# Optimization experiments

Hardware: AMD Instinct MI355X
Metric: run time of the kernel (lower is better)

Reference implementation:

```python
import jax, jax.numpy as jnp
import numpy as np

TAU = 2.0       # init_tau
VTH = 1.0       # v_threshold
VRESET = 0.0    # v_reset (hard reset)
ALPHA = 2.0     # ATan surrogate width
H = 8           # num_heads
W = 20          # attention_window
TIME_STEP = 2   # config.time_step -> global_scale uses 1000 // time_step


@jax.custom_vjp
def spike(x):
    return (x >= 0.0).astype(x.dtype)

def _spike_fwd(x):
    return (x >= 0.0).astype(x.dtype), x

def _spike_bwd(x, g):
    # ATan surrogate gradient (spikingjelly default)
    sg = (ALPHA / 2.0) / (1.0 + (jnp.pi / 2.0 * ALPHA * x) ** 2)
    return (g * sg,)

spike.defvjp(_spike_fwd, _spike_bwd)


def lif(x_seq):
    """Multi-step LIF, decay_input=False, hard reset. x_seq: [T, ...] -> spikes [T, ...]."""
    def step(v, x):
        h = v - (v - VRESET) / TAU + x          # neuronal charge (decay_input=False)
        s = spike(h - VTH)
        v_new = s * VRESET + (1.0 - s) * h      # hard reset
        return v_new, s
    _, s_seq = jax.lax.scan(step, jnp.zeros_like(x_seq[0]), x_seq)
    return s_seq


def bn(x, gamma, beta, eps=1e-5):
    # BatchNorm1d step_mode='m': stats over (T, B) per channel (training-mode stats)
    mean = x.mean(axis=(0, 1))
    var = x.var(axis=(0, 1))
    return (x - mean) * jax.lax.rsqrt(var + eps) * gamma + beta


def _shift(a, o):
    # a: [B, H, T, D]; out[..., t, :] = a[..., t + o, :], zero outside -> local band
    if o == 0:
        return a
    B_, H_, T_, D_ = a.shape
    z = jnp.zeros((B_, H_, abs(o), D_), a.dtype)
    if o > 0:
        return jnp.concatenate([a[:, :, o:, :], z], axis=2)
    return jnp.concatenate([z, a[:, :, :o, :]], axis=2)


def _forward(x, wq, wk, wv, w_mattn, w_proj, w_dw, w_pw, bn_gamma, bn_beta):
    T, B, C = x.shape
    D = C // H
    local_scale = 1.0 / np.sqrt(D * (2 * W + 1)).astype(np.float32)
    global_scale = 1.0 / np.sqrt(D * (1000 // TIME_STEP)).astype(np.float32)

    # spiking QKV: pointwise conv (kernel 1) + BN + LIF
    q = lif(bn(jnp.einsum('tbc,dc->tbd', x, wq), bn_gamma[0], bn_beta[0]))
    k = lif(bn(jnp.einsum('tbc,dc->tbd', x, wk), bn_gamma[1], bn_beta[1]))
    v = lif(bn(jnp.einsum('tbc,dc->tbd', x, wv), bn_gamma[2], bn_beta[2]))

    heads = lambda a: a.reshape(T, B, H, D).transpose(1, 2, 0, 3)   # [B,H,T,D]
    unheads = lambda a: a.transpose(2, 0, 1, 3).reshape(T, B, C)    # [T,B,C]
    qh, kh, vh = heads(q), heads(k), heads(v)

    # global spiking self-attention (no softmax): (Q K^T) V * global_scale
    attn = jnp.einsum('bhtd,bhsd->bhts', qh, kh)
    g_spk = lif(unheads(jnp.einsum('bhts,bhsd->bhtd', attn, vh) * global_scale))

    # local sliding-window attention over offsets [-W, W] (banded, no [T,T] matrix)
    out_l = jnp.zeros_like(vh)
    for o in range(-W, W + 1):
        s = jnp.einsum('bhtd,bhtd->bht', qh, _shift(kh, o))
        out_l = out_l + s[..., None] * _shift(vh, o)
    l_spk = lif(unheads(out_l * local_scale))

    # depthwise temporal conv branch on V: v_dw -> LIF -> v_pw (1x1 over heads)
    dw = jax.lax.conv_general_dilated(
        vh, w_dw, window_strides=(1, 1), padding=((4, 4), (0, 0)),
        dimension_numbers=('NCHW', 'OIHW', 'NCHW'), feature_group_count=H)
    dw_spk_h = heads(lif(unheads(dw)))
    dw_out = unheads(jnp.einsum('bhtd,gh->bgtd', dw_spk_h, w_pw))

    # merge branches, then mattn conv+BN+LIF and proj conv+BN+LIF
    y0 = lif(g_spk + l_spk + dw_out)
    y1 = lif(bn(jnp.einsum('tbc,dc->tbd', y0, w_mattn), bn_gamma[3], bn_beta[3]))
    out = lif(bn(jnp.einsum('tbc,dc->tbd', y1, w_proj), bn_gamma[4], bn_beta[4]))
    return out


def setup_inputs() -> dict:
    key = jax.random.key(0)
    ks = jax.random.split(key, 10)
    T, B, C = 500, 8, 512
    sc = 0.03
    x = jax.random.normal(ks[0], (T, B, C), jnp.float32)
    wq = jax.random.normal(ks[1], (C, C), jnp.float32) * sc
    wk = jax.random.normal(ks[2], (C, C), jnp.float32) * sc
    wv = jax.random.normal(ks[3], (C, C), jnp.float32) * sc
    w_mattn = jax.random.normal(ks[4], (C, C), jnp.float32) * sc
    w_proj = jax.random.normal(ks[5], (C, C), jnp.float32) * sc
    w_dw = jax.random.normal(ks[6], (H, 1, 9, 1), jnp.float32) * 0.3   # depthwise (9,1)
    w_pw = jax.random.normal(ks[7], (H, H), jnp.float32) * 0.3         # 1x1 over heads
    bn_gamma = jax.random.uniform(ks[8], (5, C), jnp.float32) + 0.5
    bn_beta = jax.random.normal(ks[9], (5, C), jnp.float32) * 0.1
    return {'x': x, 'wq': wq, 'wk': wk, 'wv': wv, 'w_mattn': w_mattn,
            'w_proj': w_proj, 'w_dw': w_dw, 'w_pw': w_pw,
            'bn_gamma': bn_gamma, 'bn_beta': bn_beta}


def reference(x, wq, wk, wv, w_mattn, w_proj, w_dw, w_pw, bn_gamma, bn_beta):
    return _forward(x, wq, wk, wv, w_mattn, w_proj, w_dw, w_pw, bn_gamma, bn_beta)
```

## Files before the change

### kernel.cpp

```cpp
#include <hip/hip_runtime.h>
#include <cmath>

#define TT 500
#define NTOT 2048000
#define WW 20

typedef _Float16 f16x8 __attribute__((ext_vector_type(8)));
typedef _Float16 f16x4 __attribute__((ext_vector_type(4)));
typedef float f32x4 __attribute__((ext_vector_type(4)));

#define C1SC 4.8828125e-4f
#define C2SC 2.384185791015625e-7f

__device__ __forceinline__ void gload16(const _Float16* g, _Float16* l) {
    __builtin_amdgcn_global_load_lds(
        (const __attribute__((address_space(1))) unsigned int*)g,
        (__attribute__((address_space(3))) unsigned int*)l, 16, 0, 0);
}
__device__ __forceinline__ void gload16f(const float* g, float* l) {
    __builtin_amdgcn_global_load_lds(
        (const __attribute__((address_space(1))) unsigned int*)g,
        (__attribute__((address_space(3))) unsigned int*)l, 16, 0, 0);
}
__device__ __forceinline__ void gload4b(const unsigned char* g, unsigned char* l) {
    __builtin_amdgcn_global_load_lds(
        (const __attribute__((address_space(1))) unsigned int*)g,
        (__attribute__((address_space(3))) unsigned int*)l, 4, 0, 0);
}

__global__ __launch_bounds__(256) void prep_split_k(
    const float* __restrict__ x, const float* __restrict__ wq,
    const float* __restrict__ wk, const float* __restrict__ wv,
    const float* __restrict__ wm, const float* __restrict__ wp,
    _Float16* __restrict__ X0, _Float16* __restrict__ X1, _Float16* __restrict__ X2,
    _Float16* __restrict__ Q0, _Float16* __restrict__ Q1, _Float16* __restrict__ Q2,
    _Float16* __restrict__ M0, _Float16* __restrict__ M1, _Float16* __restrict__ M2,
    _Float16* __restrict__ P0, _Float16* __restrict__ P1, _Float16* __restrict__ P2)
{
    int gid = blockIdx.x * 256 + threadIdx.x;
    const float* src;
    _Float16 *d0, *d1, *d2;
    size_t si, di;
    if (gid < 512000) {
        src = x; d0 = X0; d1 = X1; d2 = X2; si = di = (size_t)gid * 4;
    } else if (gid < 708608) {
        int g = gid - 512000;
        int s3 = g >> 16;
        src = (s3 == 0) ? wq : ((s3 == 1) ? wk : wv);
        d0 = Q0; d1 = Q1; d2 = Q2;
        si = (size_t)(g & 65535) * 4;
        di = (size_t)g * 4;
    } else if (gid < 774144) {
        int g = gid - 708608;
        src = wm; d0 = M0; d1 = M1; d2 = M2; si = di = (size_t)g * 4;
    } else {
        int g = gid - 774144;
        src = wp; d0 = P0; d1 = P1; d2 = P2; si = di = (size_t)g * 4;
    }
    float4 v = *(const float4*)(src + si);
    float f[4] = {v.x, v.y, v.z, v.w};
    f16x4 a, b, c;
#pragma unroll
    for (int i = 0; i < 4; ++i) {
        _Float16 h0 = (_Float16)f[i];
        float r1 = f[i] - (float)h0;
        _Float16 h1 = (_Float16)(r1 * 2048.0f);
        float r2 = r1 - (float)h1 * C1SC;
        _Float16 h2 = (_Float16)(r2 * 4194304.0f);
        a[i] = h0; b[i] = h1; c[i] = h2;
    }
    *(f16x4*)(d0 + di) = a;
    *(f16x4*)(d1 + di) = b;
    *(f16x4*)(d2 + di) = c;
}

__global__ __launch_bounds__(256) void gemm_f16s3_k(
    const _Float16* __restrict__ X0, const _Float16* __restrict__ X1,
    const _Float16* __restrict__ X2,
    const _Float16* __restrict__ B0g, const _Float16* __restrict__ B1g,
    const _Float16* __restrict__ B2g,
    float* __restrict__ out, float* __restrict__ colpart, int M)
{
    __shared__ __align__(16) _Float16 sA[36864];
    int tid = threadIdx.x;
    int bid = blockIdx.x;
    int xcd = bid & 7;
    int j = bid >> 3;
    int mblk = (xcd << 3) | (j & 7);
    int nblk = j >> 3;
    int mBase = mblk * 64;
    int nBase = nblk * 128;
    int wv = tid >> 6;
    int lane = tid & 63;
    int wr = wv >> 1, wc = wv & 1;
    int lg = lane >> 4, l16 = lane & 15;

    int subrow = lane >> 2;
    int s4 = lane & 3;
    int rA = (wv << 4) + subrow;
    int sl8 = (s4 ^ ((rA >> 1) & 3)) * 8;
    int mA = mBase + rA; if (mA >= M) mA = 0;
    const _Float16* gA0 = X0 + (size_t)mA * 512 + sl8;
    const _Float16* gA1 = X1 + (size_t)mA * 512 + sl8;
    const _Float16* gA2 = X2 + (size_t)mA * 512 + sl8;
    const _Float16* gB00 = B0g + (size_t)(nBase + rA) * 512 + sl8;
    const _Float16* gB01 = B0g + (size_t)(nBase + 64 + rA) * 512 + sl8;
    const _Float16* gB10 = B1g + (size_t)(nBase + rA) * 512 + sl8;
    const _Float16* gB11 = B1g + (size_t)(nBase + 64 + rA) * 512 + sl8;
    const _Float16* gB20 = B2g + (size_t)(nBase + rA) * 512 + sl8;
    const _Float16* gB21 = B2g + (size_t)(nBase + 64 + rA) * 512 + sl8;
    int wb = wv << 9;
    _Float16* lA0 = sA + wb;
    _Float16* lA1 = sA + 2048 + wb;
    _Float16* lA2 = sA + 4096 + wb;
    _Float16* lB00 = sA + 6144 + wb;
    _Float16* lB01 = sA + 8192 + wb;
    _Float16* lB10 = sA + 10240 + wb;
    _Float16* lB11 = sA + 12288 + wb;
    _Float16* lB20 = sA + 14336 + wb;
    _Float16* lB21 = sA + 16384 + wb;

    auto stage = [&](int kt, int off) {
        gload16(gA0 + kt, lA0 + off);
        gload16(gA1 + kt, lA1 + off);
        gload16(gA2 + kt, lA2 + off);
        gload16(gB00 + kt, lB00 + off);
        gload16(gB01 + kt, lB01 + off);
        gload16(gB10 + kt, lB10 + off);
        gload16(gB11 + kt, lB11 + off);
        gload16(gB20 + kt, lB20 + off);
        gload16(gB21 + kt, lB21 + off);
    };

    int sd = (lg ^ ((l16 >> 1) & 3)) * 8;

    f32x4 acc0[2][4] = {}, acc1[2][4] = {}, acc2[2][4] = {};

    stage(0, 0);
    __syncthreads();
    int cur = 0;
    for (int kt = 0; kt < 512; kt += 32) {
        int coff = cur * 18432;
        if (kt + 32 < 512) stage(kt + 32, 18432 - coff);
        f16x8 a0f[2], a1f[2], a2f[2];
#pragma unroll
        for (int i = 0; i < 2; ++i) {
            int off = (wr * 32 + i * 16 + l16) * 32 + sd + coff;
            a0f[i] = *(const f16x8*)&sA[off];
            a1f[i] = *(const f16x8*)&sA[2048 + off];
            a2f[i] = *(const f16x8*)&sA[4096 + off];
        }
#pragma unroll
        for (int jj = 0; jj < 4; ++jj) {
            int boff = 6144 + (wc * 64 + jj * 16 + l16) * 32 + sd + coff;
            f16x8 b0f = *(const f16x8*)&sA[boff];
            f16x8 b1f = *(const f16x8*)&sA[4096 + boff];
            f16x8 b2f = *(const f16x8*)&sA[8192 + boff];
#pragma unroll
            for (int i = 0; i < 2; ++i) {
                acc0[i][jj] = __builtin_amdgcn_mfma_f32_16x16x32_f16(a0f[i], b0f, acc0[i][jj], 0, 0, 0);
                acc1[i][jj] = __builtin_amdgcn_mfma_f32_16x16x32_f16(a0f[i], b1f, acc1[i][jj], 0, 0, 0);
                acc1[i][jj] = __builtin_amdgcn_mfma_f32_16x16x32_f16(a1f[i], b0f, acc1[i][jj], 0, 0, 0);
                acc2[i][jj] = __builtin_amdgcn_mfma_f32_16x16x32_f16(a1f[i], b1f, acc2[i][jj], 0, 0, 0);
                acc2[i][jj] = __builtin_amdgcn_mfma_f32_16x16x32_f16(a0f[i], b2f, acc2[i][jj], 0, 0, 0);
                acc2[i][jj] = __builtin_amdgcn_mfma_f32_16x16x32_f16(a2f[i], b0f, acc2[i][jj], 0, 0, 0);
            }
        }
        __syncthreads();
        cur ^= 1;
    }
#pragma unroll
    for (int i = 0; i < 2; ++i)
#pragma unroll
        for (int jj = 0; jj < 4; ++jj)
#pragma unroll
            for (int r = 0; r < 4; ++r)
                acc0[i][jj][r] = fmaf(C2SC, acc2[i][jj][r],
                                      fmaf(C1SC, acc1[i][jj][r], acc0[i][jj][r]));
    float* red = (float*)sA;
#pragma unroll
    for (int jj = 0; jj < 4; ++jj) {
        float s = 0.f, q = 0.f;
#pragma unroll
        for (int i = 0; i < 2; ++i)
#pragma unroll
            for (int r = 0; r < 4; ++r) {
                int mrow = mBase + wr * 32 + i * 16 + lg * 4 + r;
                float v = (mrow < M) ? acc0[i][jj][r] : 0.f;
                s += v; q = fmaf(v, v, q);
            }
        s += __shfl_xor(s, 16, 64); s += __shfl_xor(s, 32, 64);
        q += __shfl_xor(q, 16, 64); q += __shfl_xor(q, 32, 64);
        if (lane < 16) {
            int col = wc * 64 + jj * 16 + lane;
            red[(wr * 128 + col) * 2 + 0] = s;
            red[(wr * 128 + col) * 2 + 1] = q;
        }
    }
    __syncthreads();
    if (tid < 128) {
        float ss = red[tid * 2 + 0] + red[(128 + tid) * 2 + 0];
        float qq = red[tid * 2 + 1] + red[(128 + tid) * 2 + 1];
        colpart[((size_t)mblk * 1536 + nBase + tid) * 2 + 0] = ss;
        colpart[((size_t)mblk * 1536 + nBase + tid) * 2 + 1] = qq;
    }
    int wsel = nBase >> 9;
    int col0 = nBase & 511;
    float* outp = out + (size_t)wsel * NTOT;
#pragma unroll
    for (int i = 0; i < 2; ++i) {
        int m0 = mBase + wr * 32 + i * 16 + lg * 4;
#pragma unroll
        for (int jj = 0; jj < 4; ++jj) {
            int cc = col0 + wc * 64 + jj * 16 + l16;
#pragma unroll
            for (int r = 0; r < 4; ++r) {
                int m = m0 + r;
                if (m < M) outp[(size_t)m * 512 + cc] = acc0[i][jj][r];
            }
        }
    }
}

__global__ __launch_bounds__(256) void gemm_hs3_k(
    const _Float16* __restrict__ Ah,
    const _Float16* __restrict__ B0g, const _Float16* __restrict__ B1g,
    const _Float16* __restrict__ B2g,
    float* __restrict__ out, float* __restrict__ colpart, int M)
{
    __shared__ __align__(16) _Float16 sH[16384];
    int tid = threadIdx.x;
    int bid = blockIdx.x;
    int xcd = bid & 7;
    int j = bid >> 3;
    int mblk = (xcd << 3) | (j & 7);
    int nblk = j >> 3;
    int mBase = mblk * 64;
    int col0 = nblk * 64;
    int wv = tid >> 6;
    int lane = tid & 63;
    int wr = wv >> 1, wc = wv & 1;
    int lg = lane >> 4, l16 = lane & 15;

    int subrow = lane >> 2;
    int s4 = lane & 3;
    int rA = (wv << 4) + subrow;
    int sl8 = (s4 ^ ((rA >> 1) & 3)) * 8;
    int mA = mBase + rA; if (mA >= M) mA = 0;
    const _Float16* gA  = Ah  + (size_t)mA * 512 + sl8;
    const _Float16* gB0 = B0g + (size_t)(col0 + rA) * 512 + sl8;
    const _Float16* gB1 = B1g + (size_t)(col0 + rA) * 512 + sl8;
    const _Float16* gB2 = B2g + (size_t)(col0 + rA) * 512 + sl8;
    int wb = wv << 9;
    _Float16* lA  = sH + wb;
    _Float16* lB0 = sH + 2048 + wb;
    _Float16* lB1 = sH + 4096 + wb;
    _Float16* lB2 = sH + 6144 + wb;

    auto stage = [&](int kt, int off) {
        gload16(gA + kt, lA + off);
        gload16(gB0 + kt, lB0 + off);
        gload16(gB1 + kt, lB1 + off);
        gload16(gB2 + kt, lB2 + off);
    };

    int sd = (lg ^ ((l16 >> 1) & 3)) * 8;

    f32x4 acc0[2][2] = {}, acc1[2][2] = {}, acc2[2][2] = {};

    stage(0, 0);
    __syncthreads();
    int cur = 0;
    for (int kt = 0; kt < 512; kt += 32) {
        int coff = cur * 8192;
        if (kt + 32 < 512) stage(kt + 32, 8192 - coff);
        f16x8 af[2];
#pragma unroll
        for (int i = 0; i < 2; ++i)
            af[i] = *(const f16x8*)&sH[(wr * 32 + i * 16 + l16) * 32 + sd + coff];
#pragma unroll
        for (int jj = 0; jj < 2; ++jj) {
            int boff = 2048 + (wc * 32 + jj * 16 + l16) * 32 + sd + coff;
            f16x8 b0f = *(const f16x8*)&sH[boff];
            f16x8 b1f = *(const f16x8*)&sH[2048 + boff];
            f16x8 b2f = *(const f16x8*)&sH[4096 + boff];
#pragma unroll
            for (int i = 0; i < 2; ++i) {
                acc0[i][jj] = __builtin_amdgcn_mfma_f32_16x16x32_f16(af[i], b0f, acc0[i][jj], 0, 0, 0);
                acc1[i][jj] = __builtin_amdgcn_mfma_f32_16x16x32_f16(af[i], b1f, acc1[i][jj], 0, 0, 0);
                acc2[i][jj] = __builtin_amdgcn_mfma_f32_16x16x32_f16(af[i], b2f, acc2[i][jj], 0, 0, 0);
            }
        }
        __syncthreads();
        cur ^= 1;
    }
#pragma unroll
    for (int i = 0; i < 2; ++i)
#pragma unroll
        for (int jj = 0; jj < 2; ++jj)
#pragma unroll
            for (int r = 0; r < 4; ++r)
                acc0[i][jj][r] = fmaf(C2SC, acc2[i][jj][r],
                                      fmaf(C1SC, acc1[i][jj][r], acc0[i][jj][r]));
    float* red = (float*)sH;
#pragma unroll
    for (int jj = 0; jj < 2; ++jj) {
        float s = 0.f, q = 0.f;
#pragma unroll
        for (int i = 0; i < 2; ++i)
#pragma unroll
            for (int r = 0; r < 4; ++r) {
                int mrow = mBase + wr * 32 + i * 16 + lg * 4 + r;
                float v = (mrow < M) ? acc0[i][jj][r] : 0.f;
                s += v; q = fmaf(v, v, q);
            }
        s += __shfl_xor(s, 16, 64); s += __shfl_xor(s, 32, 64);
        q += __shfl_xor(q, 16, 64); q += __shfl_xor(q, 32, 64);
        if (lane < 16) {
            int col = wc * 32 + jj * 16 + lane;
            red[(wr * 64 + col) * 2 + 0] = s;
            red[(wr * 64 + col) * 2 + 1] = q;
        }
    }
    __syncthreads();
    if (tid < 64) {
        float ss = red[tid * 2 + 0] + red[(64 + tid) * 2 + 0];
        float qq = red[tid * 2 + 1] + red[(64 + tid) * 2 + 1];
        colpart[((size_t)mblk * 512 + col0 + tid) * 2 + 0] = ss;
        colpart[((size_t)mblk * 512 + col0 + tid) * 2 + 1] = qq;
    }
#pragma unroll
    for (int i = 0; i < 2; ++i) {
        int m0 = mBase + wr * 32 + i * 16 + lg * 4;
#pragma unroll
        for (int jj = 0; jj < 2; ++jj) {
            int cc = col0 + wc * 32 + jj * 16 + l16;
#pragma unroll
            for (int r = 0; r < 4; ++r) {
                int m = m0 + r;
                if (m < M) out[(size_t)m * 512 + cc] = acc0[i][jj][r];
            }
        }
    }
}

__global__ __launch_bounds__(256) void lif_seg_k(
    const float* __restrict__ pre, const float* __restrict__ colpart, int CT, int chunks,
    const float* __restrict__ gamma, const float* __restrict__ beta,
    float* __restrict__ outF, unsigned char* __restrict__ outB,
    _Float16* __restrict__ outH, int segLen, int warm)
{
    int gid = blockIdx.x * 256 + threadIdx.x;
    int tensor = gid >> 12;
    int bc = gid & 4095;
    int ch = (tensor << 9) | (bc & 511);
    double s = 0.0, s2 = 0.0;
    for (int k = 0; k < chunks; ++k) {
        s  += (double)colpart[((size_t)k * CT + ch) * 2 + 0];
        s2 += (double)colpart[((size_t)k * CT + ch) * 2 + 1];
    }
    double mean = s / 4000.0;
    double var = s2 / 4000.0 - mean * mean;
    double scd = (double)gamma[ch] / sqrt(var + 1e-5);
    float sc = (float)scd;
    float sh = (float)((double)beta[ch] - mean * scd);
    const float* q0 = pre + (size_t)tensor * NTOT + bc;
    float* oF = outF ? outF + (size_t)tensor * NTOT + bc : nullptr;
    unsigned char* oB = outB ? outB + (size_t)tensor * NTOT + bc : nullptr;
    _Float16* oH = outH ? outH + (size_t)tensor * NTOT + bc : nullptr;
    int t0 = blockIdx.y * segLen;
    int twarm = (t0 - warm > 0) ? (t0 - warm) : 0;
    int tend = (t0 + segLen < TT) ? (t0 + segLen) : TT;
    float v = 0.f;
    float b0[8];
#pragma unroll
    for (int j = 0; j < 8; ++j) {
        int tt = twarm + j;
        b0[j] = (tt < tend) ? q0[(size_t)tt * 4096] : 0.f;
    }
    for (int t = twarm; t < tend; t += 8) {
        float n0[8];
#pragma unroll
        for (int j = 0; j < 8; ++j) {
            int tt = t + 8 + j;
            n0[j] = (tt < tend) ? q0[(size_t)tt * 4096] : 0.f;
        }
#pragma unroll
        for (int j = 0; j < 8; ++j) {
            int tc = t + j;
            if (tc >= tend) break;
            float bnx = fmaf(b0[j], sc, sh);
            float h = fmaf(0.5f, v, bnx);
            float sp = (h >= 1.f) ? 1.f : 0.f;
            v = (h >= 1.f) ? 0.f : h;
            if (tc >= t0) {
                if (oB)      oB[(size_t)tc * 4096] = (unsigned char)sp;
                else if (oH) oH[(size_t)tc * 4096] = (_Float16)sp;
                else         oF[(size_t)tc * 4096] = sp;
            }
        }
#pragma unroll
        for (int j = 0; j < 8; ++j) b0[j] = n0[j];
    }
}

__global__ __launch_bounds__(256) void ktv_part_k(
    const unsigned char* __restrict__ kspk, const unsigned char* __restrict__ vspk,
    float* __restrict__ part)
{
    __shared__ __align__(16) float kb[16][64], vb[16][64];
    int bh = blockIdx.x;
    int seg = blockIdx.y;
    int t0p = seg * 125, t1p = t0p + 125;
    int b = bh >> 3, h = bh & 7;
    int tid = threadIdx.x;
    int d1b = (tid >> 4) * 4, d2b = (tid & 15) * 4;
    size_t cb = (size_t)b * 512 + h * 64;
    int sRow = tid >> 4;
    int sD = (tid & 15) * 4;
    float acc[4][4] = {};
    uchar4 pk, pv;
    auto preload = [&](int tt) {
        int t = tt + sRow;
        if (t < t1p) {
            pk = *(const uchar4*)(kspk + (size_t)t * 4096 + cb + sD);
            pv = *(const uchar4*)(vspk + (size_t)t * 4096 + cb + sD);
        } else {
            pk = make_uchar4(0, 0, 0, 0); pv = make_uchar4(0, 0, 0, 0);
        }
    };
    preload(t0p);
    for (int tt = t0p; tt < t1p; tt += 16) {
        __syncthreads();
        kb[sRow][sD + 0] = (float)pk.x; kb[sRow][sD + 1] = (float)pk.y;
        kb[sRow][sD + 2] = (float)pk.z; kb[sRow][sD + 3] = (float)pk.w;
        vb[sRow][sD + 0] = (float)pv.x; vb[sRow][sD + 1] = (float)pv.y;
        vb[sRow][sD + 2] = (float)pv.z; vb[sRow][sD + 3] = (float)pv.w;
        __syncthreads();
        preload(tt + 16);
#pragma unroll
        for (int tl = 0; tl < 16; ++tl) {
            float4 k4 = *(const float4*)&kb[tl][d1b];
            float4 v4 = *(const float4*)&vb[tl][d2b];
            float ka[4] = {k4.x, k4.y, k4.z, k4.w};
            float va[4] = {v4.x, v4.y, v4.z, v4.w};
#pragma unroll
            for (int i = 0; i < 4; ++i)
#pragma unroll
                for (int j = 0; j < 4; ++j)
                    acc[i][j] = fmaf(ka[i], va[j], acc[i][j]);
        }
    }
    size_t ob = ((size_t)seg * 64 + bh) * 4096;
#pragma unroll
    for (int i = 0; i < 4; ++i)
        *(float4*)(part + ob + (size_t)(d1b + i) * 64 + d2b) =
            make_float4(acc[i][0], acc[i][1], acc[i][2], acc[i][3]);
}

__global__ __launch_bounds__(256) void ktv_reduce_k(
    const float* __restrict__ part, float* __restrict__ ktv)
{
    int i4 = (blockIdx.x * 256 + threadIdx.x) * 4;
    float4 a = *(const float4*)(part + i4);
    float4 b = *(const float4*)(part + 262144 + i4);
    float4 c = *(const float4*)(part + 2 * 262144 + i4);
    float4 d = *(const float4*)(part + 3 * 262144 + i4);
    *(float4*)(ktv + i4) = make_float4(((a.x + b.x) + c.x) + d.x,
                                       ((a.y + b.y) + c.y) + d.y,
                                       ((a.z + b.z) + c.z) + d.z,
                                       ((a.w + b.w) + c.w) + d.w);
}

__global__ __launch_bounds__(256) void gapply_t_k(
    const unsigned char* __restrict__ sq, const float* __restrict__ ktv,
    float* __restrict__ gpre, float gscale)
{
    __shared__ float qs[10][512];
    int tid = threadIdx.x;
    int t0 = blockIdx.x * 10;
    int b = blockIdx.y;
    for (int i = tid; i < 1280; i += 256) {
        int t = i >> 7;
        int c4 = (i & 127) * 4;
        uchar4 u = *(const uchar4*)(sq + (size_t)(t0 + t) * 4096 + b * 512 + c4);
        qs[t][c4 + 0] = (float)u.x; qs[t][c4 + 1] = (float)u.y;
        qs[t][c4 + 2] = (float)u.z; qs[t][c4 + 3] = (float)u.w;
    }
    __syncthreads();
#pragma unroll
    for (int half = 0; half < 2; ++half) {
        int c = tid + half * 256;
        int h = c >> 6, dcol = c & 63;
        const float* kt = ktv + ((size_t)(b * 8 + h) * 64) * 64 + dcol;
        float acc[10] = {};
        for (int d1 = 0; d1 < 64; ++d1) {
            float kv = kt[(size_t)d1 * 64];
#pragma unroll
            for (int t = 0; t < 10; ++t)
                acc[t] = fmaf(qs[t][h * 64 + d1], kv, acc[t]);
        }
#pragma unroll
        for (int t = 0; t < 10; ++t)
            gpre[(size_t)(t0 + t) * 4096 + b * 512 + c] = acc[t] * gscale;
    }
}

__global__ __launch_bounds__(256) void local_k(
    const unsigned char* __restrict__ qspk, const unsigned char* __restrict__ kspk,
    const unsigned char* __restrict__ vspk, float* __restrict__ lpre, float lscale)
{
    __shared__ __align__(16) float qs[32][68];
    __shared__ __align__(16) float ks[72][68];
    __shared__ __align__(16) float vs[72][68];
    __shared__ float sm[32][72];
    int t0 = blockIdx.x * 32;
    int bh = blockIdx.y;
    int b = bh >> 3, h = bh & 7;
    int tid = threadIdx.x;
    size_t cb = (size_t)b * 512 + h * 64;

    for (int i = tid; i < 512; i += 256) {
        int r = i >> 4, d4 = (i & 15) * 4;
        int t = t0 + r;
        if (t < TT) {
            uchar4 u = *(const uchar4*)(qspk + (size_t)t * 4096 + cb + d4);
            qs[r][d4 + 0] = (float)u.x; qs[r][d4 + 1] = (float)u.y;
            qs[r][d4 + 2] = (float)u.z; qs[r][d4 + 3] = (float)u.w;
        } else {
            qs[r][d4 + 0] = 0.f; qs[r][d4 + 1] = 0.f; qs[r][d4 + 2] = 0.f; qs[r][d4 + 3] = 0.f;
        }
    }
    for (int i = tid; i < 1152; i += 256) {
        int r = i >> 4, d4 = (i & 15) * 4;
        int u_ = t0 - WW + r;
        if (u_ >= 0 && u_ < TT) {
            uchar4 uk = *(const uchar4*)(kspk + (size_t)u_ * 4096 + cb + d4);
            uchar4 uv = *(const uchar4*)(vspk + (size_t)u_ * 4096 + cb + d4);
            ks[r][d4 + 0] = (float)uk.x; ks[r][d4 + 1] = (float)uk.y;
            ks[r][d4 + 2] = (float)uk.z; ks[r][d4 + 3] = (float)uk.w;
            vs[r][d4 + 0] = (float)uv.x; vs[r][d4 + 1] = (float)uv.y;
            vs[r][d4 + 2] = (float)uv.z; vs[r][d4 + 3] = (float)uv.w;
        } else {
            ks[r][d4 + 0] = 0.f; ks[r][d4 + 1] = 0.f; ks[r][d4 + 2] = 0.f; ks[r][d4 + 3] = 0.f;
            vs[r][d4 + 0] = 0.f; vs[r][d4 + 1] = 0.f; vs[r][d4 + 2] = 0.f; vs[r][d4 + 3] = 0.f;
        }
    }
    __syncthreads();

    int tA = tid >> 3;
    int ug = tid & 7;
    float4 qreg[16];
#pragma unroll
    for (int i = 0; i < 16; ++i) qreg[i] = *(const float4*)&qs[tA][i * 4];
#pragma unroll
    for (int ui = 0; ui < 9; ++ui) {
        int u = ug + ui * 8;
        float acc = 0.f;
#pragma unroll
        for (int i = 0; i < 16; ++i) {
            float4 k4 = *(const float4*)&ks[u][i * 4];
            acc = fmaf(qreg[i].x, k4.x, acc);
            acc = fmaf(qreg[i].y, k4.y, acc);
            acc = fmaf(qreg[i].z, k4.z, acc);
            acc = fmaf(qreg[i].w, k4.w, acc);
        }
        sm[tA][u] = acc;
    }
    __syncthreads();

#pragma unroll
    for (int oi = 0; oi < 2; ++oi) {
        int idx = tid + oi * 256;
        int t = idx >> 4;
        int dg = (idx & 15) * 4;
        float4 acc = make_float4(0.f, 0.f, 0.f, 0.f);
        for (int o = 0; o < 41; ++o) {
            int u = t + o;
            float s = sm[t][u];
            float4 v4 = *(const float4*)&vs[u][dg];
            acc.x = fmaf(s, v4.x, acc.x);
            acc.y = fmaf(s, v4.y, acc.y);
            acc.z = fmaf(s, v4.z, acc.z);
            acc.w = fmaf(s, v4.w, acc.w);
        }
        int tg = t0 + t;
        if (tg < TT) {
            acc.x *= lscale; acc.y *= lscale; acc.z *= lscale; acc.w *= lscale;
            *(float4*)(lpre + (size_t)tg * 4096 + cb + dg) = acc;
        }
    }
}

__global__ __launch_bounds__(256) void branch_y0_k(
    const float* __restrict__ gpre, const float* __restrict__ lpre,
    const unsigned char* __restrict__ sv, const float* __restrict__ wdw,
    const float* __restrict__ wpw, _Float16* __restrict__ sy0,
    int segLen, int warm)
{
    __shared__ __align__(16) float gb[2][8][256];
    __shared__ __align__(16) float lb[2][8][256];
    __shared__ __align__(16) unsigned char vbuf[2][8][256];
    int tid = threadIdx.x;
    int wave = tid >> 6, lane = tid & 63;
    int gw0 = blockIdx.x * 4;
    int b = gw0 >> 3;
    int dg0 = gw0 & 7;
    int h = lane >> 3, dl = lane & 7;
    int dg = dg0 + wave;
    int c = h * 64 + dg * 8 + dl;
    int base = b * 512 + c;
    int p = h * 32 + (((wave + h) & 3) << 3) + dl;

    int rowS[2], gcol[2];
#pragma unroll
    for (int v = 0; v < 2; ++v) {
        int f = tid + (v << 8);
        rowS[v] = f >> 6;
        int jj = f & 63;
        int hj = jj >> 3;
        int sj = (jj >> 1) & 3;
        int wj = (sj - hj) & 3;
        gcol[v] = b * 512 + hj * 64 + dg0 * 8 + (wj << 3) + ((jj & 1) << 2);
    }

    float w9[9];
#pragma unroll
    for (int j = 0; j < 9; ++j) w9[j] = wdw[h * 9 + j];
    float w8[8];
#pragma unroll
    for (int j = 0; j < 8; ++j) w8[j] = wpw[h * 8 + j];
    int t0 = blockIdx.y * segLen;
    int twarm = (t0 - warm > 0) ? (t0 - warm) : 0;
    int tend = (t0 + segLen < TT) ? (t0 + segLen) : TT;

    auto stageGL = [&](int ct, int bi) {
#pragma unroll
        for (int v = 0; v < 2; ++v) {
            size_t ga = (size_t)(ct + rowS[v]) * 4096 + gcol[v];
            int lo = (v << 10) + (wave << 8);
            gload16f(gpre + ga, &gb[bi][0][0] + lo);
            gload16f(lpre + ga, &lb[bi][0][0] + lo);
        }
    };
    auto stageV = [&](int ct, int bi) {
#pragma unroll
        for (int v = 0; v < 2; ++v) {
            size_t ga = (size_t)(ct + rowS[v]) * 4096 + gcol[v];
            int lo = (v << 10) + (wave << 8);
            gload4b(sv + ga, &vbuf[bi][0][0] + lo);
        }
    };

    float vg = 0.f, vl = 0.f, vd = 0.f, vy = 0.f;
    float win[12];
#pragma unroll
    for (int i = 0; i < 12; ++i) {
        int tt = twarm - 4 + i;
        win[i] = (tt >= 0 && tt < TT) ? (float)sv[(size_t)tt * 4096 + base] : 0.f;
    }
    stageGL(twarm, 0);
    stageV(twarm + 8, 0);
    __syncthreads();
    int cur = 0;
    for (int T0 = twarm; T0 < tend; T0 += 8) {
        if (T0 + 8 < tend) { stageGL(T0 + 8, cur ^ 1); stageV(T0 + 16, cur ^ 1); }
#pragma unroll
        for (int r = 0; r < 8; ++r) {
            int tc = T0 + r;
            if (tc >= tend) break;
            float cg = gb[cur][r][p];
            float cl = lb[cur][r][p];
            float nv = (tc + 8 < TT) ? (float)vbuf[cur][r][p] : 0.f;
            float x = 0.f;
#pragma unroll
            for (int q = 0; q < 9; ++q) x = fmaf(w9[q], win[q], x);
            float hd = fmaf(0.5f, vd, x);
            float sd = (hd >= 1.f) ? 1.f : 0.f;
            vd = (hd >= 1.f) ? 0.f : hd;
            float hg = fmaf(0.5f, vg, cg);
            float sg = (hg >= 1.f) ? 1.f : 0.f;
            vg = (hg >= 1.f) ? 0.f : hg;
            float hl = fmaf(0.5f, vl, cl);
            float sl = (hl >= 1.f) ? 1.f : 0.f;
            vl = (hl >= 1.f) ? 0.f : hl;
            float mix = 0.f;
#pragma unroll
            for (int h2 = 0; h2 < 8; ++h2)
                mix = fmaf(w8[h2], __shfl(sd, h2 * 8 + dl, 64), mix);
            float xy = (sg + sl) + mix;
            float hy = fmaf(0.5f, vy, xy);
            float sy = (hy >= 1.f) ? 1.f : 0.f;
            vy = (hy >= 1.f) ? 0.f : hy;
            if (tc >= t0) sy0[(size_t)tc * 4096 + base] = (_Float16)sy;
#pragma unroll
            for (int i2 = 0; i2 < 11; ++i2) win[i2] = win[i2 + 1];
            win[11] = nv;
        }
        __syncthreads();
        cur ^= 1;
    }
}

extern "C" void kernel_launch(void* const* d_in, const int* in_sizes, int n_in,
                              void* d_out, int out_size, void* d_ws, size_t ws_size,
                              hipStream_t stream)
{
    const float* x       = (const float*)d_in[0];
    const float* wq      = (const float*)d_in[1];
    const float* wk      = (const float*)d_in[2];
    const float* wv      = (const float*)d_in[3];
    const float* w_mattn = (const float*)d_in[4];
    const float* w_proj  = (const float*)d_in[5];
    const float* w_dw    = (const float*)d_in[6];
    const float* w_pw    = (const float*)d_in[7];
    const float* bn_g    = (const float*)d_in[8];
    const float* bn_b    = (const float*)d_in[9];
    float* out = (float*)d_out;
    float* ws = (float*)d_ws;

    float gs32 = (float)std::sqrt((double)(64 * 500));
    float gscale = (float)(1.0 / (double)gs32);
    float ls32 = (float)std::sqrt((double)(64 * 41));
    float lscale = (float)(1.0 / (double)ls32);
    const int M = TT * 8;

    float* S0 = ws;
    float* S1 = ws + (size_t)NTOT;
    float* S2 = ws + 2 * (size_t)NTOT;
    float* part4   = ws + 3 * (size_t)NTOT;
    float* ktvBuf  = part4 + 4 * 262144;
    float* colpart = ktvBuf + 262144;
    unsigned char* spk = (unsigned char*)(colpart + 196608);
    unsigned char* sq  = spk;
    unsigned char* sk  = spk + (size_t)NTOT;
    unsigned char* sv  = spk + 2 * (size_t)NTOT;
    _Float16* sy0h = (_Float16*)(spk + 3 * (size_t)NTOT);
    _Float16* sy1h = (_Float16*)spk;
    _Float16* X0 = (_Float16*)spk;
    _Float16* X1 = X0 + (size_t)NTOT;
    _Float16* X2 = X1 + (size_t)NTOT;
    _Float16* Wm0 = (_Float16*)(spk + 6 * (size_t)NTOT);
    _Float16* Wm1 = Wm0 + 262144;
    _Float16* Wm2 = Wm1 + 262144;
    _Float16* Wp0 = Wm2 + 262144;
    _Float16* Wp1 = Wp0 + 262144;
    _Float16* Wp2 = Wp1 + 262144;
    _Float16* Wq0 = (_Float16*)part4;
    _Float16* Wq1 = Wq0 + 786432;
    _Float16* Wq2 = Wq1 + 786432;

    prep_split_k<<<3280, 256, 0, stream>>>(x, wq, wk, wv, w_mattn, w_proj,
                                           X0, X1, X2, Wq0, Wq1, Wq2,
                                           Wm0, Wm1, Wm2, Wp0, Wp1, Wp2);
    gemm_f16s3_k<<<768, 256, 0, stream>>>(X0, X1, X2, Wq0, Wq1, Wq2, S0, colpart, M);
    lif_seg_k<<<dim3(48, 10), 256, 0, stream>>>(S0, colpart, 1536, 64, bn_g, bn_b,
                                                nullptr, sq, nullptr, 50, 64);
    ktv_part_k<<<dim3(64, 4), 256, 0, stream>>>(sk, sv, part4);
    ktv_reduce_k<<<256, 256, 0, stream>>>(part4, ktvBuf);
    gapply_t_k<<<dim3(50, 8), 256, 0, stream>>>(sq, ktvBuf, S0, gscale);
    local_k<<<dim3(16, 64), 256, 0, stream>>>(sq, sk, sv, S1, lscale);
    branch_y0_k<<<dim3(16, 20), 256, 0, stream>>>(S0, S1, sv, w_dw, w_pw, sy0h, 25, 64);
    gemm_hs3_k<<<512, 256, 0, stream>>>(sy0h, Wm0, Wm1, Wm2, S2, colpart, M);
    lif_seg_k<<<dim3(16, 20), 256, 0, stream>>>(S2, colpart, 512, 64, bn_g + 1536,
                                                bn_b + 1536, nullptr, nullptr, sy1h, 25, 64);
    gemm_hs3_k<<<512, 256, 0, stream>>>(sy1h, Wp0, Wp1, Wp2, S0, colpart, M);
    lif_seg_k<<<dim3(16, 20), 256, 0, stream>>>(S0, colpart, 512, 64, bn_g + 2048,
                                                bn_b + 2048, out, nullptr, nullptr, 25, 64);

    (void)in_sizes; (void)n_in; (void)out_size; (void)ws_size;
}
```

Before: 315.4 us.

## Triple-buffer fp16 split GEMM LDS loads and vectorize global-apply LDS reads

The three-way split-fp16 GEMM moves from a double buffer to a triple-buffered LDS ring. Each step issues loads two stages ahead, waits with vmcnt(4) and uses a single barrier per k-step instead of two, so global loads overlap more with MFMA work. Separately, the global attention apply kernel unrolls the d1 loop by 4 and reads q values as float4 from LDS. The changes use more LDS, which may lower occupancy, and depend on hand-placed waitcnt counts being correct.

```diff
diff --git a/kernel.cpp b/kernel.cpp
--- a/kernel.cpp
+++ b/kernel.cpp
@@ -228,7 +228,7 @@
     const _Float16* __restrict__ B2g,
     float* __restrict__ out, float* __restrict__ colpart, int M)
 {
-    __shared__ __align__(16) _Float16 sH[16384];
+    __shared__ __align__(16) _Float16 sH[24576];
     int tid = threadIdx.x;
     int bid = blockIdx.x;
     int xcd = bid & 7;
@@ -252,28 +252,19 @@
     const _Float16* gB1 = B1g + (size_t)(col0 + rA) * 512 + sl8;
     const _Float16* gB2 = B2g + (size_t)(col0 + rA) * 512 + sl8;
     int wb = wv << 9;
-    _Float16* lA  = sH + wb;
-    _Float16* lB0 = sH + 2048 + wb;
-    _Float16* lB1 = sH + 4096 + wb;
-    _Float16* lB2 = sH + 6144 + wb;
 
     auto stage = [&](int kt, int off) {
-        gload16(gA + kt, lA + off);
-        gload16(gB0 + kt, lB0 + off);
-        gload16(gB1 + kt, lB1 + off);
-        gload16(gB2 + kt, lB2 + off);
+        gload16(gA + kt, sH + off + wb);
+        gload16(gB0 + kt, sH + off + 2048 + wb);
+        gload16(gB1 + kt, sH + off + 4096 + wb);
+        gload16(gB2 + kt, sH + off + 6144 + wb);
     };
 
     int sd = (lg ^ ((l16 >> 1) & 3)) * 8;
 
     f32x4 acc0[2][2] = {}, acc1[2][2] = {}, acc2[2][2] = {};
 
-    stage(0, 0);
-    __syncthreads();
-    int cur = 0;
-    for (int kt = 0; kt < 512; kt += 32) {
-        int coff = cur * 8192;
-        if (kt + 32 < 512) stage(kt + 32, 8192 - coff);
+    auto compute = [&](int coff) {
         f16x8 af[2];
 #pragma unroll
         for (int i = 0; i < 2; ++i)
@@ -291,9 +282,28 @@
                 acc2[i][jj] = __builtin_amdgcn_mfma_f32_16x16x32_f16(af[i], b2f, acc2[i][jj], 0, 0, 0);
             }
         }
-        __syncthreads();
-        cur ^= 1;
-    }
+    };
+
+    stage(0, 0);
+    stage(32, 8192);
+    int offC = 0, offS = 16384;
+    for (int n = 0; n < 14; ++n) {
+        asm volatile("s_waitcnt vmcnt(4)" ::: "memory");
+        __builtin_amdgcn_s_barrier();
+        stage((n + 2) * 32, offS);
+        compute(offC);
+        offC += 8192; if (offC == 24576) offC = 0;
+        offS += 8192; if (offS == 24576) offS = 0;
+    }
+    asm volatile("s_waitcnt vmcnt(4)" ::: "memory");
+    __builtin_amdgcn_s_barrier();
+    compute(offC);
+    offC += 8192; if (offC == 24576) offC = 0;
+    asm volatile("s_waitcnt vmcnt(0)" ::: "memory");
+    __builtin_amdgcn_s_barrier();
+    compute(offC);
+    __syncthreads();
+
 #pragma unroll
     for (int i = 0; i < 2; ++i)
 #pragma unroll
@@ -476,7 +486,7 @@
     const unsigned char* __restrict__ sq, const float* __restrict__ ktv,
     float* __restrict__ gpre, float gscale)
 {
-    __shared__ float qs[10][512];
+    __shared__ __align__(16) float qs[10][512];
     int tid = threadIdx.x;
     int t0 = blockIdx.x * 10;
     int b = blockIdx.y;
@@ -494,11 +504,19 @@
         int h = c >> 6, dcol = c & 63;
         const float* kt = ktv + ((size_t)(b * 8 + h) * 64) * 64 + dcol;
         float acc[10] = {};
-        for (int d1 = 0; d1 < 64; ++d1) {
-            float kv = kt[(size_t)d1 * 64];
-#pragma unroll
-            for (int t = 0; t < 10; ++t)
-                acc[t] = fmaf(qs[t][h * 64 + d1], kv, acc[t]);
+        for (int d1b = 0; d1b < 64; d1b += 4) {
+            float kv0 = kt[(size_t)(d1b + 0) * 64];
+            float kv1 = kt[(size_t)(d1b + 1) * 64];
+            float kv2 = kt[(size_t)(d1b + 2) * 64];
+            float kv3 = kt[(size_t)(d1b + 3) * 64];
+#pragma unroll
+            for (int t = 0; t < 10; ++t) {
+                float4 q4 = *(const float4*)&qs[t][h * 64 + d1b];
+                acc[t] = fmaf(q4.x, kv0, acc[t]);
+                acc[t] = fmaf(q4.y, kv1, acc[t]);
+                acc[t] = fmaf(q4.z, kv2, acc[t]);
+                acc[t] = fmaf(q4.w, kv3, acc[t]);
+            }
         }
 #pragma unroll
         for (int t = 0; t < 10; ++t)
```

New measurement: 311.5 us. About the same (-1.3%).
